# Kernel tuning notes

Measured on AMD Instinct MI355X. Metric: run time of the kernel, lower is better.

The kernel has to match this reference:

```python
import jax, jax.numpy as jnp
import numpy as np

B, NUM_PEAKS, PEAK_SIZE = 2, 64, 1000
MOTIF, HID, DEPTH, PROF_K = 640, 256, 7, 75


def conv1d(x, w, b, dilation=1):
    # x: (N, C, L), w: (O, I, K), valid padding
    out = jax.lax.conv_general_dilated(
        x, w, window_strides=(1,), padding='VALID',
        rhs_dilation=(dilation,), dimension_numbers=('NCH', 'OIH', 'NCH'))
    return out + b[None, :, None]


def setup_inputs() -> dict:
    key = jax.random.key(0)
    ks = jax.random.split(key, 10)
    L = NUM_PEAKS * PEAK_SIZE
    x = jax.random.normal(ks[0], (B, L, MOTIF), dtype=jnp.float32)
    peak_split = jnp.full((B * NUM_PEAKS,), PEAK_SIZE, dtype=jnp.int64) if jax.config.jax_enable_x64 else jnp.full((B * NUM_PEAKS,), PEAK_SIZE, dtype=jnp.int32)
    n_peaks = jnp.full((B,), NUM_PEAKS, dtype=jnp.int32)
    # parameters (kaiming-ish small init)
    w_proj = jax.random.normal(ks[1], (HID, MOTIF, 1), dtype=jnp.float32) / np.sqrt(MOTIF)
    b_proj = jnp.zeros((HID,), jnp.float32)
    w_dil = jax.random.normal(ks[2], (DEPTH, HID, HID, 3), dtype=jnp.float32) / np.sqrt(3 * HID)
    b_dil = jnp.zeros((DEPTH, HID), jnp.float32)
    w_prof = jax.random.normal(ks[3], (1, HID, PROF_K), dtype=jnp.float32) / np.sqrt(PROF_K * HID)
    b_prof = jnp.zeros((1,), jnp.float32)
    w_atpm = jax.random.normal(ks[4], (1, HID), dtype=jnp.float32) / np.sqrt(HID)
    b_atpm = jnp.zeros((1,), jnp.float32)
    return {
        'x': x, 'peak_split': peak_split, 'n_peaks': n_peaks, 'max_n_peaks': NUM_PEAKS,
        'w_proj': w_proj, 'b_proj': b_proj, 'w_dil': w_dil, 'b_dil': b_dil,
        'w_prof': w_prof, 'b_prof': b_prof, 'w_atpm': w_atpm, 'b_atpm': b_atpm,
    }


def reference(x, peak_split, n_peaks, max_n_peaks,
              w_proj, b_proj, w_dil, b_dil, w_prof, b_prof, w_atpm, b_atpm):
    # fast path: all samples have max_n_peaks uniform-size peaks
    batch, length, _ = x.shape
    num_peaks = int(np.asarray(n_peaks)[0])
    peak_size = length // num_peaks
    # 1x1 motif projection: (B, L, MOTIF) -> (B, HID, L)
    h = conv1d(jnp.transpose(x, (0, 2, 1)), w_proj, b_proj)
    # split into peaks: (B*num_peaks, HID, peak_size)
    h = jnp.transpose(h, (0, 2, 1)).reshape(batch * num_peaks, peak_size, HID)
    h = jnp.transpose(h, (0, 2, 1))
    # dilated conv tower with residual crop
    for i in range(DEPTH):
        dilation = 2 ** (i + 1)
        out = conv1d(h, w_dil[i], b_dil[i], dilation=dilation)
        crop = (h.shape[-1] - out.shape[-1]) // 2
        h = jax.nn.relu(out) + h[..., crop:-crop]
    peak_atpm = h.mean(axis=2)                      # (N, HID)
    peak_profile = conv1d(h, w_prof, b_prof)        # (N, 1, out_len)
    peak_atpm = jax.nn.softplus(peak_atpm @ w_atpm.T + b_atpm)
    peak_atpm = peak_atpm.reshape(batch, num_peaks, 1)
    peak_profile = jax.nn.softplus(peak_profile.reshape(batch, -1))
    return (peak_atpm, peak_profile)
```

## Files before the change

kernel.cpp:

```cpp
#include <hip/hip_runtime.h>
#include <hip/hip_bf16.h>
#include <math.h>

#define HID 256
#define MOTIF 640
#define PEAK 1000
#define NPEAKS 128
#define DEPTHN 7
#define PROFK 75
#define FINLEN 492
#define PROFLEN 418

typedef unsigned short u16;
typedef unsigned int u32;
typedef _Float16 f16x8 __attribute__((ext_vector_type(8)));
typedef float f32x16 __attribute__((ext_vector_type(16)));

__device__ __forceinline__ u16 f2h(float f) {
    _Float16 h = (_Float16)f; u16 b; __builtin_memcpy(&b, &h, 2); return b;
}
__device__ __forceinline__ float h2f(u16 b) {
    _Float16 h; __builtin_memcpy(&h, &b, 2); return (float)h;
}
__device__ __forceinline__ float hlo(u32 u) { return h2f((u16)(u & 0xffff)); }
__device__ __forceinline__ float hhi(u32 u) { return h2f((u16)(u >> 16)); }
__device__ __forceinline__ u32 pk2h(float a, float b) {
    return (u32)f2h(a) | ((u32)f2h(b) << 16);
}

__device__ __forceinline__ void gll16(const void* g, void* l) {
    __builtin_amdgcn_global_load_lds(
        (const __attribute__((address_space(1))) void*)g,
        (__attribute__((address_space(3))) void*)l, 16, 0, 0);
}

__global__ __launch_bounds__(256) void conv_wdil_all(const float* __restrict__ w,
                                                     u16* __restrict__ wf,
                                                     float* __restrict__ zp) {
    const int layer = blockIdx.y;
    int i = blockIdx.x * 256 + threadIdx.x;
    if (layer == 0 && i < NPEAKS) zp[i] = 0.f;
    const float* wl = w + (size_t)layer * HID * HID * 3;
    u16* wfl = wf + (size_t)layer * (3 * HID * HID);
    int cil = i & 15; int j = i >> 4;
    int c = j & 255; j >>= 8;
    int ci16 = j & 15; int k = j >> 4;
    wfl[i] = f2h(wl[((size_t)c * HID + ci16 * 16 + cil) * 3 + k]);
}

__global__ __launch_bounds__(256) void conv_wproj(const float* __restrict__ w,
                                                  u16* __restrict__ wf) {
    int i = blockIdx.x * 256 + threadIdx.x;
    if (i >= MOTIF * HID) return;
    int ml = i & 15;
    int c = (i >> 4) & 255;
    int m16 = i >> 12;
    wf[i] = f2h(w[(size_t)c * MOTIF + m16 * 16 + ml]);
}

template<int TAPS, int KCI, int CCI, int DIL, bool SRCF32, bool RESID, bool ATPM>
__global__ __launch_bounds__(256, 3) void mfma_gemm(
    const void* __restrict__ src, int in_len, int in_stride,
    const u16* __restrict__ wf, const float* __restrict__ bias,
    u16* __restrict__ dst, int out_len,
    const float* __restrict__ watpm, float* part)
{
    constexpr int R    = 128 + (TAPS - 1) * DIL;
    constexpr int GR   = CCI / 8;
    constexpr int SUBS = CCI / 16;
    constexpr int KTC  = TAPS * SUBS;
    constexpr int NC   = KCI / CCI;
    constexpr int ASLOTS = KTC * 256;
    constexpr int AIT  = KTC;
    constexpr int BSLOTS = R * GR;
    constexpr int BIT  = (BSLOTS + 255) / 256;
    constexpr int NIF  = SRCF32 ? AIT : (AIT + BIT);

    __shared__ __attribute__((aligned(16))) u16 As[2][ASLOTS * 8];
    __shared__ __attribute__((aligned(16))) u16 Bs[2][(BSLOTS + 64) * 8];
    __shared__ float aw[4];
    const int tid = threadIdx.x;
    const int wave = tid >> 6, lane = tid & 63;
    const int col = lane & 31, half = lane >> 5;
    const int cg = wave & 1, tg = wave >> 1;
    const int t0 = blockIdx.x * 128;
    const int c0 = blockIdx.y * 128;
    const int n  = blockIdx.z;

    const float* snf = (const float*)src + (size_t)n * in_len * in_stride;
    const u16*   snh = (const u16*)src + (size_t)n * in_len * in_stride;

    f32x16 acc[2][2];
    #pragma unroll
    for (int cs = 0; cs < 2; ++cs)
        #pragma unroll
        for (int ts = 0; ts < 2; ++ts)
            #pragma unroll
            for (int q = 0; q < 16; ++q) acc[cs][ts][q] = 0.f;

    auto stageA = [&](int cc, int b) {
        const int kt0 = (cc * CCI) >> 4;
        #pragma unroll
        for (int it = 0; it < AIT; ++it) {
            const int s = it * 256 + tid;
            const int ktl = s >> 8;
            const int c = (s & 255) >> 1, hf = s & 1;
            const int k = ktl / SUBS, sub = ktl % SUBS;
            const int ktg = k * (KCI / 16) + kt0 + sub;
            gll16(wf + (size_t)(ktg * 256 + c0 + c) * 16 + hf * 8,
                  &As[b][(size_t)s * 8]);
        }
    };
    auto stageB = [&](int cc, int b) {
        const int ci0 = cc * CCI;
        #pragma unroll
        for (int it = 0; it < BIT; ++it) {
            int s = it * 256 + tid;
            if (s >= BSLOTS) s = BSLOTS - 1;
            const int r = s / GR, ch = s % GR;
            int g = t0 + r; if (g > in_len - 1) g = in_len - 1;
            const int chs = ch ^ (r & (GR - 1));
            if (SRCF32) {
                const float* p = snf + (size_t)g * in_stride + ci0 + chs * 8;
                float4 a = *(const float4*)p;
                float4 bq = *(const float4*)(p + 4);
                uint4 o;
                o.x = pk2h(a.x, a.y); o.y = pk2h(a.z, a.w);
                o.z = pk2h(bq.x, bq.y); o.w = pk2h(bq.z, bq.w);
                *(uint4*)&Bs[b][(size_t)s * 8] = o;
            } else {
                gll16(snh + (size_t)g * in_stride + ci0 + chs * 8,
                      &Bs[b][(size_t)s * 8]);
            }
        }
    };
    auto compute = [&](int b) {
        #pragma unroll
        for (int k = 0; k < TAPS; ++k) {
            #pragma unroll
            for (int sub = 0; sub < SUBS; ++sub) {
                const int ktl = k * SUBS + sub;
                f16x8 bf[2];
                #pragma unroll
                for (int ts = 0; ts < 2; ++ts) {
                    const int row = tg * 64 + ts * 32 + col + k * DIL;
                    const int sl = row * GR + ((sub * 2 + half) ^ (row & (GR - 1)));
                    bf[ts] = *reinterpret_cast<const f16x8*>(&Bs[b][(size_t)sl * 8]);
                }
                #pragma unroll
                for (int cs = 0; cs < 2; ++cs) {
                    const f16x8 af = *reinterpret_cast<const f16x8*>(
                        &As[b][(size_t)(ktl * 256 + (cg * 64 + cs * 32 + col) * 2 + half) * 8]);
                    acc[cs][0] = __builtin_amdgcn_mfma_f32_32x32x16_f16(af, bf[0], acc[cs][0], 0, 0, 0);
                    acc[cs][1] = __builtin_amdgcn_mfma_f32_32x32x16_f16(af, bf[1], acc[cs][1], 0, 0, 0);
                }
            }
        }
    };

    if (SRCF32) { stageB(0, 0); stageA(0, 0); stageB(1, 1); stageA(1, 1); }
    else        { stageA(0, 0); stageB(0, 0); stageA(1, 1); stageB(1, 1); }

    #pragma unroll
    for (int c = 0; c < NC; ++c) {
        if (SRCF32) asm volatile("s_waitcnt lgkmcnt(0)" ::: "memory");
        if (c + 1 < NC) asm volatile("s_waitcnt vmcnt(%0)" :: "i"(NIF) : "memory");
        else            asm volatile("s_waitcnt vmcnt(0)" ::: "memory");
        __builtin_amdgcn_s_barrier();
        asm volatile("" ::: "memory");
        compute(c & 1);
        asm volatile("" ::: "memory");
        __builtin_amdgcn_s_barrier();
        asm volatile("" ::: "memory");
        if (c + 2 < NC) {
            if (SRCF32) { stageB(c + 2, c & 1); stageA(c + 2, c & 1); }
            else        { stageA(c + 2, c & 1); stageB(c + 2, c & 1); }
        }
    }

    float apart = 0.f;
    #pragma unroll
    for (int ts = 0; ts < 2; ++ts) {
        const int t = t0 + tg * 64 + ts * 32 + col;
        if (t >= out_len) continue;
        const float* resf = snf + (size_t)(t + DIL) * in_stride;
        const u16*   resh = snh + (size_t)(t + DIL) * in_stride;
        u16* oh = dst + ((size_t)n * out_len + t) * HID;
        #pragma unroll
        for (int cs = 0; cs < 2; ++cs) {
            #pragma unroll
            for (int g = 0; g < 4; ++g) {
                const int c = c0 + cg * 64 + cs * 32 + g * 8 + half * 4;
                float4 bv = *(const float4*)(bias + c);
                float v0 = acc[cs][ts][g * 4 + 0] + bv.x;
                float v1 = acc[cs][ts][g * 4 + 1] + bv.y;
                float v2 = acc[cs][ts][g * 4 + 2] + bv.z;
                float v3 = acc[cs][ts][g * 4 + 3] + bv.w;
                if (RESID) {
                    if (SRCF32) {
                        float4 r = *(const float4*)(resf + c);
                        v0 = fmaxf(v0, 0.f) + r.x;
                        v1 = fmaxf(v1, 0.f) + r.y;
                        v2 = fmaxf(v2, 0.f) + r.z;
                        v3 = fmaxf(v3, 0.f) + r.w;
                    } else {
                        uint2 r = *(const uint2*)(resh + c);
                        v0 = fmaxf(v0, 0.f) + hlo(r.x);
                        v1 = fmaxf(v1, 0.f) + hhi(r.x);
                        v2 = fmaxf(v2, 0.f) + hlo(r.y);
                        v3 = fmaxf(v3, 0.f) + hhi(r.y);
                    }
                }
                if (ATPM) {
                    float4 wv = *(const float4*)(watpm + c);
                    apart += v0 * wv.x + v1 * wv.y + v2 * wv.z + v3 * wv.w;
                }
                uint2 o; o.x = pk2h(v0, v1); o.y = pk2h(v2, v3);
                *(uint2*)(oh + c) = o;
            }
        }
    }
    if (ATPM) {
        #pragma unroll
        for (int off = 32; off; off >>= 1) apart += __shfl_down(apart, off, 64);
        if (lane == 0) aw[wave] = apart;
        __syncthreads();
        if (tid == 0) atomicAdd(part + n, aw[0] + aw[1] + aw[2] + aw[3]);
    }
}

__global__ void atpm_fin(const float* __restrict__ part,
                         const float* __restrict__ batpm, float* __restrict__ out) {
    int i = threadIdx.x;
    float tot = part[i] / (float)FINLEN + batpm[0];
    out[i] = fmaxf(tot, 0.f) + log1pf(expf(-fabsf(tot)));
}

__global__ __launch_bounds__(256) void prof_kernel(
    const u16* __restrict__ h, const float* __restrict__ wprof,
    const float* __restrict__ bprof, float* __restrict__ out)
{
    __shared__ __attribute__((aligned(16))) float hs[64 * 204];
    __shared__ float red[128 * 8];
    const int tid = threadIdx.x;
    const int wave = tid >> 6, lane = tid & 63;
    const int ts = lane & 31, hw = lane >> 5;
    const int cig = wave * 2 + hw;
    const int n = blockIdx.y, t0 = blockIdx.x * 128;
    const u16* hn = h + (size_t)n * FINLEN * HID;
    float acc[4] = {0.f, 0.f, 0.f, 0.f};

    for (int ci0 = 0; ci0 < HID; ci0 += 64) {
        __syncthreads();
        {
            const int ci = tid & 63, rg = tid >> 6;
            for (int base = 0; base < 204; base += 16) {
                const int r0 = base + rg * 4;
                if (r0 >= 204) continue;
                float4 v;
                float* vp = (float*)&v;
                #pragma unroll
                for (int j = 0; j < 4; ++j) {
                    int g = t0 + r0 + j; if (g > FINLEN - 1) g = FINLEN - 1;
                    vp[j] = h2f(hn[(size_t)g * HID + ci0 + ci]);
                }
                *(float4*)&hs[ci * 204 + r0] = v;
            }
        }
        __syncthreads();
        for (int ci = 0; ci < 8; ++ci) {
            const int cia = cig * 8 + ci;
            const float4* hrow = (const float4*)&hs[cia * 204];
            const float* wrow = wprof + (size_t)(ci0 + cia) * PROFK;
            float wqf[84];
            #pragma unroll
            for (int q = 0; q < 3; ++q) wqf[q] = 0.f;
            #pragma unroll
            for (int q = 78; q < 84; ++q) wqf[q] = 0.f;
            #pragma unroll
            for (int k = 0; k < PROFK; ++k) wqf[k + 3] = wrow[k];
            #pragma unroll
            for (int m = 0; m < 20; ++m) {
                float4 h4 = hrow[ts + m];
                const float* hp = (const float*)&h4;
                #pragma unroll
                for (int j = 0; j < 4; ++j) {
                    #pragma unroll
                    for (int a = 0; a < 4; ++a) {
                        acc[a] += wqf[4 * m + j - a + 3] * hp[j];
                    }
                }
            }
        }
    }
    #pragma unroll
    for (int a = 0; a < 4; ++a) red[(ts * 4 + a) * 8 + cig] = acc[a];
    __syncthreads();
    if (tid < 128) {
        float s = 0.f;
        #pragma unroll
        for (int c8 = 0; c8 < 8; ++c8) s += red[tid * 8 + c8];
        const int t = t0 + tid;
        if (t < PROFLEN) {
            float v = s + bprof[0];
            out[(size_t)n * PROFLEN + t] = fmaxf(v, 0.f) + log1pf(expf(-fabsf(v)));
        }
    }
}

extern "C" void kernel_launch(void* const* d_in, const int* in_sizes, int n_in,
                              void* d_out, int out_size, void* d_ws, size_t ws_size,
                              hipStream_t stream) {
    const float* x     = (const float*)d_in[0];
    const float* wproj = (const float*)d_in[4];
    const float* bproj = (const float*)d_in[5];
    const float* wdil  = (const float*)d_in[6];
    const float* bdil  = (const float*)d_in[7];
    const float* wprof = (const float*)d_in[8];
    const float* bprof = (const float*)d_in[9];
    const float* watpm = (const float*)d_in[10];
    const float* batpm = (const float*)d_in[11];
    float* outAtpm = (float*)d_out;
    float* outProf = outAtpm + NPEAKS;

    char* ws = (char*)d_ws;
    u16* hA    = (u16*)ws;
    u16* hB    = (u16*)(ws + 65536000);
    u16* wpf   = (u16*)(ws + 131072000);
    u16* wslot = (u16*)(ws + 131399680);
    float* part = (float*)(ws + 134152192);

    conv_wproj<<<(MOTIF * HID + 255) / 256, 256, 0, stream>>>(wproj, wpf);
    conv_wdil_all<<<dim3(768, DEPTHN), 256, 0, stream>>>(wdil, wslot, part);

    mfma_gemm<1, MOTIF, 32, 0, true, false, false><<<dim3(8, 2, NPEAKS), 256, 0, stream>>>(
        x, PEAK, MOTIF, wpf, bproj, hA, PEAK, nullptr, nullptr);

    #define LAYER(i, DIL, SRC, DST, INL, OUTL, TT)                                              \
        mfma_gemm<3, HID, 16, DIL, false, true, false><<<dim3(TT, 2, NPEAKS), 256, 0, stream>>>( \
            SRC, INL, HID, wslot + (size_t)(i) * (3 * HID * HID),                               \
            bdil + (size_t)(i) * HID, DST, OUTL, nullptr, nullptr);
    LAYER(0,   2, hA, hB, 1000, 996, 8)
    LAYER(1,   4, hB, hA,  996, 988, 8)
    LAYER(2,   8, hA, hB,  988, 972, 8)
    LAYER(3,  16, hB, hA,  972, 940, 8)
    LAYER(4,  32, hA, hB,  940, 876, 7)
    LAYER(5,  64, hB, hA,  876, 748, 6)
    #undef LAYER
    mfma_gemm<3, HID, 16, 128, false, true, true><<<dim3(4, 2, NPEAKS), 256, 0, stream>>>(
        hA, 748, HID, wslot + (size_t)6 * (3 * HID * HID), bdil + (size_t)6 * HID,
        hB, 492, watpm, part);

    atpm_fin<<<1, 128, 0, stream>>>(part, batpm, outAtpm);
    prof_kernel<<<dim3(4, NPEAKS), 256, 0, stream>>>(hB, wprof, bprof, outProf);
}
```

Measured before the change: 1.155 ms.

## Parameterize MFMA GEMM wave layout and use larger 512-thread tiles

Templatizes the MFMA conv/GEMM kernel on the number of waves along the channel and time axes. The projection now uses one 512-thread block covering all 256 output channels, so each x tile is converted from fp32 and staged only once. Dilated layers 0-4 use 256-position time tiles, which amortizes the dilation halo and weight staging over more columns. Blocks get bigger and use more LDS, which could lower occupancy and add tail imbalance.

```diff
diff --git a/kernel.cpp b/kernel.cpp
--- a/kernel.cpp
+++ b/kernel.cpp
@@ -58,33 +58,38 @@
     wf[i] = f2h(w[(size_t)c * MOTIF + m16 * 16 + ml]);
 }
 
-template<int TAPS, int KCI, int CCI, int DIL, bool SRCF32, bool RESID, bool ATPM>
-__global__ __launch_bounds__(256, 3) void mfma_gemm(
+template<int NWC, int NWT, int TAPS, int KCI, int CCI, int DIL,
+         bool SRCF32, bool RESID, bool ATPM>
+__global__ __launch_bounds__(NWC * NWT * 64, (NWC * NWT == 8) ? 4 : 3)
+void mfma_gemm(
     const void* __restrict__ src, int in_len, int in_stride,
     const u16* __restrict__ wf, const float* __restrict__ bias,
     u16* __restrict__ dst, int out_len,
     const float* __restrict__ watpm, float* part)
 {
-    constexpr int R    = 128 + (TAPS - 1) * DIL;
+    constexpr int BS   = NWC * NWT * 64;
+    constexpr int CW   = NWC * 64;
+    constexpr int TW   = NWT * 64;
+    constexpr int R    = TW + (TAPS - 1) * DIL;
     constexpr int GR   = CCI / 8;
     constexpr int SUBS = CCI / 16;
     constexpr int KTC  = TAPS * SUBS;
     constexpr int NC   = KCI / CCI;
-    constexpr int ASLOTS = KTC * 256;
-    constexpr int AIT  = KTC;
+    constexpr int ASLOTS = KTC * CW * 2;
+    constexpr int AIT  = (ASLOTS + BS - 1) / BS;
     constexpr int BSLOTS = R * GR;
-    constexpr int BIT  = (BSLOTS + 255) / 256;
+    constexpr int BIT  = (BSLOTS + BS - 1) / BS;
     constexpr int NIF  = SRCF32 ? AIT : (AIT + BIT);
 
-    __shared__ __attribute__((aligned(16))) u16 As[2][ASLOTS * 8];
+    __shared__ __attribute__((aligned(16))) u16 As[2][(ASLOTS + 64) * 8];
     __shared__ __attribute__((aligned(16))) u16 Bs[2][(BSLOTS + 64) * 8];
-    __shared__ float aw[4];
+    __shared__ float aw[NWC * NWT];
     const int tid = threadIdx.x;
     const int wave = tid >> 6, lane = tid & 63;
     const int col = lane & 31, half = lane >> 5;
-    const int cg = wave & 1, tg = wave >> 1;
-    const int t0 = blockIdx.x * 128;
-    const int c0 = blockIdx.y * 128;
+    const int cg = wave % NWC, tg = wave / NWC;
+    const int t0 = blockIdx.x * TW;
+    const int c0 = blockIdx.y * CW;
     const int n  = blockIdx.z;
 
     const float* snf = (const float*)src + (size_t)n * in_len * in_stride;
@@ -102,9 +107,11 @@
         const int kt0 = (cc * CCI) >> 4;
         #pragma unroll
         for (int it = 0; it < AIT; ++it) {
-            const int s = it * 256 + tid;
-            const int ktl = s >> 8;
-            const int c = (s & 255) >> 1, hf = s & 1;
+            int s = it * BS + tid;
+            if (s >= ASLOTS) s = ASLOTS - 1;
+            const int ktl = s / (CW * 2);
+            const int rem = s % (CW * 2);
+            const int c = rem >> 1, hf = rem & 1;
             const int k = ktl / SUBS, sub = ktl % SUBS;
             const int ktg = k * (KCI / 16) + kt0 + sub;
             gll16(wf + (size_t)(ktg * 256 + c0 + c) * 16 + hf * 8,
@@ -115,7 +122,7 @@
         const int ci0 = cc * CCI;
         #pragma unroll
         for (int it = 0; it < BIT; ++it) {
-            int s = it * 256 + tid;
+            int s = it * BS + tid;
             if (s >= BSLOTS) s = BSLOTS - 1;
             const int r = s / GR, ch = s % GR;
             int g = t0 + r; if (g > in_len - 1) g = in_len - 1;
@@ -150,7 +157,7 @@
                 #pragma unroll
                 for (int cs = 0; cs < 2; ++cs) {
                     const f16x8 af = *reinterpret_cast<const f16x8*>(
-                        &As[b][(size_t)(ktl * 256 + (cg * 64 + cs * 32 + col) * 2 + half) * 8]);
+                        &As[b][(size_t)(ktl * (CW * 2) + (cg * 64 + cs * 32 + col) * 2 + half) * 8]);
                     acc[cs][0] = __builtin_amdgcn_mfma_f32_32x32x16_f16(af, bf[0], acc[cs][0], 0, 0, 0);
                     acc[cs][1] = __builtin_amdgcn_mfma_f32_32x32x16_f16(af, bf[1], acc[cs][1], 0, 0, 0);
                 }
@@ -225,7 +232,12 @@
         for (int off = 32; off; off >>= 1) apart += __shfl_down(apart, off, 64);
         if (lane == 0) aw[wave] = apart;
         __syncthreads();
-        if (tid == 0) atomicAdd(part + n, aw[0] + aw[1] + aw[2] + aw[3]);
+        if (tid == 0) {
+            float s = 0.f;
+            #pragma unroll
+            for (int wv = 0; wv < NWC * NWT; ++wv) s += aw[wv];
+            atomicAdd(part + n, s);
+        }
     }
 }
 
@@ -333,21 +345,27 @@
     conv_wproj<<<(MOTIF * HID + 255) / 256, 256, 0, stream>>>(wproj, wpf);
     conv_wdil_all<<<dim3(768, DEPTHN), 256, 0, stream>>>(wdil, wslot, part);
 
-    mfma_gemm<1, MOTIF, 32, 0, true, false, false><<<dim3(8, 2, NPEAKS), 256, 0, stream>>>(
+    mfma_gemm<4, 2, 1, MOTIF, 32, 0, true, false, false>
+        <<<dim3(8, 1, NPEAKS), 512, 0, stream>>>(
         x, PEAK, MOTIF, wpf, bproj, hA, PEAK, nullptr, nullptr);
 
-    #define LAYER(i, DIL, SRC, DST, INL, OUTL, TT)                                              \
-        mfma_gemm<3, HID, 16, DIL, false, true, false><<<dim3(TT, 2, NPEAKS), 256, 0, stream>>>( \
-            SRC, INL, HID, wslot + (size_t)(i) * (3 * HID * HID),                               \
+    #define LAYER(i, DIL, SRC, DST, INL, OUTL, TT)                                 \
+        mfma_gemm<2, 4, 3, HID, 16, DIL, false, true, false>                       \
+            <<<dim3(TT, 2, NPEAKS), 512, 0, stream>>>(                             \
+            SRC, INL, HID, wslot + (size_t)(i) * (3 * HID * HID),                  \
             bdil + (size_t)(i) * HID, DST, OUTL, nullptr, nullptr);
-    LAYER(0,   2, hA, hB, 1000, 996, 8)
-    LAYER(1,   4, hB, hA,  996, 988, 8)
-    LAYER(2,   8, hA, hB,  988, 972, 8)
-    LAYER(3,  16, hB, hA,  972, 940, 8)
-    LAYER(4,  32, hA, hB,  940, 876, 7)
-    LAYER(5,  64, hB, hA,  876, 748, 6)
+    LAYER(0,   2, hA, hB, 1000, 996, 4)
+    LAYER(1,   4, hB, hA,  996, 988, 4)
+    LAYER(2,   8, hA, hB,  988, 972, 4)
+    LAYER(3,  16, hB, hA,  972, 940, 4)
+    LAYER(4,  32, hA, hB,  940, 876, 4)
     #undef LAYER
-    mfma_gemm<3, HID, 16, 128, false, true, true><<<dim3(4, 2, NPEAKS), 256, 0, stream>>>(
+    mfma_gemm<2, 2, 3, HID, 16, 64, false, true, false>
+        <<<dim3(6, 2, NPEAKS), 256, 0, stream>>>(
+        hB, 876, HID, wslot + (size_t)5 * (3 * HID * HID), bdil + (size_t)5 * HID,
+        hA, 748, nullptr, nullptr);
+    mfma_gemm<2, 2, 3, HID, 16, 128, false, true, true>
+        <<<dim3(4, 2, NPEAKS), 256, 0, stream>>>(
         hA, 748, HID, wslot + (size_t)6 * (3 * HID * HID), bdil + (size_t)6 * HID,
         hB, 492, watpm, part);
 
```

Measured after the change: 1.181 ms. 1.02x slower.
